# Kernel optimization log

Measured on AMD Instinct MI355X. Metric: run time of the kernel, lower is better.

## Reference

```python
import jax, jax.numpy as jnp
import numpy as np

IN_FEATURES = 256
OUT_FEATURES = 128
ALPHA = 0.2  # LeakyReLU negative slope
NEG_INF = -9e15
N_NODES = 8192


def _xavier_uniform(key, shape, gain):
    fan_in, fan_out = shape[0], shape[1]
    limit = gain * np.sqrt(6.0 / (fan_in + fan_out))
    return jax.random.uniform(key, shape, jnp.float32, -limit, limit)


def setup_inputs() -> dict:
    key = jax.random.key(0)
    k_h, k_adj, k_W, k_a = jax.random.split(key, 4)
    h = jax.random.normal(k_h, (N_NODES, IN_FEATURES), dtype=jnp.float32)
    adj = jax.random.randint(k_adj, (N_NODES, N_NODES), 0, 2, dtype=jnp.int32)
    W = _xavier_uniform(k_W, (IN_FEATURES, OUT_FEATURES), gain=1.414)
    a = _xavier_uniform(k_a, (2 * OUT_FEATURES, 1), gain=1.414)
    return {"h": h, "adj": adj, "W": W, "a": a}


def reference(h, adj, W, a):
    # Wh: (N, F_out)
    Wh = h @ W
    # Decompose a = [a1; a2]; e_ij = leakyrelu(Wh_i . a1 + Wh_j . a2)
    # == the original concat([Wh_i, Wh_j]) @ a, without the O(N^2*2F) tensor.
    a1 = a[:OUT_FEATURES, 0]  # (F_out,)
    a2 = a[OUT_FEATURES:, 0]  # (F_out,)
    src = Wh @ a1  # (N,)
    dst = Wh @ a2  # (N,)
    e = jax.nn.leaky_relu(src[:, None] + dst[None, :], negative_slope=ALPHA)  # (N, N)
    attention = jnp.where(adj > 0, e, NEG_INF)
    attention = jax.nn.softmax(attention, axis=1)
    # dropout p=0.0 (eval) -> identity
    h_prime = attention @ Wh  # (N, F_out)
    return jax.nn.elu(h_prime)  # concat=True
```

## Files before the change

kernel.cpp:

```cpp
#include <hip/hip_runtime.h>

#define N_NODES 8192
#define IN_F    256
#define OUT_F   128
#define ALPHA_S 0.2f

typedef __attribute__((ext_vector_type(8))) short  short8;
typedef __attribute__((ext_vector_type(4))) short  short4v;
typedef __attribute__((ext_vector_type(4))) float  floatx4;
typedef __attribute__((ext_vector_type(4))) int    intx4;
typedef __attribute__((ext_vector_type(4))) float  fx4;

static __device__ __forceinline__ float bf2f(short s) {
    union { unsigned int i; float f; } u;
    u.i = ((unsigned int)(unsigned short)s) << 16;
    return u.f;
}
static __device__ __forceinline__ short f2bf(float f) {
    union { float f; unsigned int i; } u; u.f = f;
    unsigned int r = u.i + 0x7FFFu + ((u.i >> 16) & 1u);
    return (short)(r >> 16);
}

__global__ __launch_bounds__(512) void k_wh(
    const float* __restrict__ h, const float* __restrict__ W,
    const float* __restrict__ a,
    short* __restrict__ WhB, float* __restrict__ src, float* __restrict__ dst)
{
    __shared__ short Wt[OUT_F][IN_F + 8];
    __shared__ short htile[32][IN_F + 8];
    __shared__ float q1s[IN_F], q2s[IN_F];
    __shared__ short wh_t[OUT_F][40];

    const int t      = threadIdx.x;
    const int lane   = t & 63;
    const int wave   = t >> 6;
    const int r_base = blockIdx.x * 32;

#pragma unroll
    for (int rep = 0; rep < 4; ++rep) {
        const int idx = rep * 8192 + t * 16;
        const int k   = idx >> 7;
        const int f   = idx & 127;
        fx4 w0 = *(const fx4*)(W + idx);
        fx4 w1 = *(const fx4*)(W + idx + 4);
        fx4 w2 = *(const fx4*)(W + idx + 8);
        fx4 w3 = *(const fx4*)(W + idx + 12);
        fx4 a10 = *(const fx4*)(a + f);
        fx4 a11 = *(const fx4*)(a + f + 4);
        fx4 a12 = *(const fx4*)(a + f + 8);
        fx4 a13 = *(const fx4*)(a + f + 12);
        fx4 a20 = *(const fx4*)(a + OUT_F + f);
        fx4 a21 = *(const fx4*)(a + OUT_F + f + 4);
        fx4 a22 = *(const fx4*)(a + OUT_F + f + 8);
        fx4 a23 = *(const fx4*)(a + OUT_F + f + 12);
        float p1 = 0.f, p2 = 0.f;
#pragma unroll
        for (int e = 0; e < 4; ++e) {
            p1 = fmaf(w0[e], a10[e], p1); p2 = fmaf(w0[e], a20[e], p2);
            p1 = fmaf(w1[e], a11[e], p1); p2 = fmaf(w1[e], a21[e], p2);
            p1 = fmaf(w2[e], a12[e], p1); p2 = fmaf(w2[e], a22[e], p2);
            p1 = fmaf(w3[e], a13[e], p1); p2 = fmaf(w3[e], a23[e], p2);
        }
#pragma unroll
        for (int e = 0; e < 4; ++e) {
            Wt[f + e][k]      = f2bf(w0[e]);
            Wt[f + 4 + e][k]  = f2bf(w1[e]);
            Wt[f + 8 + e][k]  = f2bf(w2[e]);
            Wt[f + 12 + e][k] = f2bf(w3[e]);
        }
#pragma unroll
        for (int m = 1; m < 8; m <<= 1) {
            p1 += __shfl_xor(p1, m, 64);
            p2 += __shfl_xor(p2, m, 64);
        }
        if ((t & 7) == 0) { q1s[k] = p1; q2s[k] = p2; }
    }

    const int r0   = t >> 4;
    const int fgrp = t & 15;
    const int k0   = fgrp * 16;
    fx4 h0, h1, h2, h3;
    {
        const float* hp = h + (size_t)(r_base + r0) * IN_F + k0;
        h0 = *(const fx4*)hp; h1 = *(const fx4*)(hp + 4);
        h2 = *(const fx4*)(hp + 8); h3 = *(const fx4*)(hp + 12);
        short8 b0, b1;
#pragma unroll
        for (int e = 0; e < 4; ++e) {
            b0[e]     = f2bf(h0[e]); b0[4 + e] = f2bf(h1[e]);
            b1[e]     = f2bf(h2[e]); b1[4 + e] = f2bf(h3[e]);
        }
        *(short8*)&htile[r0][k0]     = b0;
        *(short8*)&htile[r0][k0 + 8] = b1;
    }
    __syncthreads();

    {
        float sp = 0.f, dp = 0.f;
#pragma unroll
        for (int e = 0; e < 4; ++e) {
            sp = fmaf(h0[e], q1s[k0 + e], sp);      dp = fmaf(h0[e], q2s[k0 + e], dp);
            sp = fmaf(h1[e], q1s[k0 + 4 + e], sp);  dp = fmaf(h1[e], q2s[k0 + 4 + e], dp);
            sp = fmaf(h2[e], q1s[k0 + 8 + e], sp);  dp = fmaf(h2[e], q2s[k0 + 8 + e], dp);
            sp = fmaf(h3[e], q1s[k0 + 12 + e], sp); dp = fmaf(h3[e], q2s[k0 + 12 + e], dp);
        }
#pragma unroll
        for (int m = 1; m < 16; m <<= 1) {
            sp += __shfl_xor(sp, m, 64);
            dp += __shfl_xor(dp, m, 64);
        }
        if (fgrp == 0) { src[r_base + r0] = sp; dst[r_base + r0] = dp; }
    }

    const int ln15 = lane & 15;
    const int q    = lane >> 4;
    const int f0   = wave * 16;
    floatx4 c0 = {0.f, 0.f, 0.f, 0.f};
    floatx4 c1 = {0.f, 0.f, 0.f, 0.f};
#pragma unroll
    for (int s = 0; s < 8; ++s) {
        short8 bf  = *(const short8*)&Wt[f0 + ln15][s * 32 + q * 8];
        short8 a0f = *(const short8*)&htile[ln15][s * 32 + q * 8];
        short8 a1f = *(const short8*)&htile[16 + ln15][s * 32 + q * 8];
        c0 = __builtin_amdgcn_mfma_f32_16x16x32_bf16(a0f, bf, c0, 0, 0, 0);
        c1 = __builtin_amdgcn_mfma_f32_16x16x32_bf16(a1f, bf, c1, 0, 0, 0);
    }
    {
        short4v p0, p1;
#pragma unroll
        for (int r = 0; r < 4; ++r) { p0[r] = f2bf(c0[r]); p1[r] = f2bf(c1[r]); }
        *(short4v*)&wh_t[f0 + ln15][q * 4]      = p0;
        *(short4v*)&wh_t[f0 + ln15][16 + q * 4] = p1;
    }
    __syncthreads();
    {
        const int ft2 = t >> 6;
        const int l2  = t & 63;
        const int n2  = l2 & 15;
        const int q2  = l2 >> 4;
        short8 v = *(const short8*)&wh_t[ft2 * 16 + n2][q2 * 8];
        *(short8*)(WhB + (((size_t)blockIdx.x * 8 + ft2) * 64 + l2) * 8) = v;
    }
}

__global__ __launch_bounds__(256) void k_weights(
    const int*   __restrict__ adj,
    const float* __restrict__ src,
    const float* __restrict__ dstv,
    short* __restrict__ P,
    float* __restrict__ denom_part)
{
    __shared__ float wsum[4];
    const int bi  = blockIdx.x;
    const int row = bi >> 1;
    const int c0  = (bi & 1) * 4096;
    const int t   = threadIdx.x;
    const int col = c0 + t * 16;

    const float srow = src[row];
    const int*   ap = adj + (size_t)row * N_NODES + col;
    const float* dp = dstv + col;

    intx4 m[4]; fx4 d[4];
#pragma unroll
    for (int v = 0; v < 4; ++v) {
        m[v] = *(const intx4*)(ap + v * 4);
        d[v] = *(const fx4*)(dp + v * 4);
    }

    short8 w0, w1;
    float lsum = 0.f;
#pragma unroll
    for (int v = 0; v < 4; ++v) {
#pragma unroll
        for (int e = 0; e < 4; ++e) {
            float x = srow + d[v][e];
            float l = fmaxf(x, ALPHA_S * x);
            short b = (m[v][e] > 0) ? f2bf(__expf(l)) : (short)0;
            lsum += bf2f(b);
            if (v < 2) w0[v * 4 + e] = b;
            else       w1[(v - 2) * 4 + e] = b;
        }
    }
    short* pp = P + (size_t)row * N_NODES + col;
    *(short8*)pp       = w0;
    *(short8*)(pp + 8) = w1;

#pragma unroll
    for (int s = 1; s < 64; s <<= 1) lsum += __shfl_xor(lsum, s, 64);
    if ((t & 63) == 0) wsum[t >> 6] = lsum;
    __syncthreads();
    if (t == 0)
        denom_part[(size_t)(bi & 1) * N_NODES + row] =
            wsum[0] + wsum[1] + wsum[2] + wsum[3];
}

#define KSPLIT 8
#define KCH  (N_NODES / KSPLIT)
#define PBK  128
#define PSTR (PBK + 8)
#define PNIT (KCH / PBK)

__global__ __launch_bounds__(512) void k_pv(
    const short* __restrict__ P,
    const short* __restrict__ WhB,
    float* __restrict__ numer_part)
{
    __shared__ short atile[128 * PSTR];

    const int t    = threadIdx.x;
    const int lane = t & 63;
    const int wave = t >> 6;
    const int rg   = blockIdx.x >> 3;
    const int kc   = blockIdx.x & 7;
    const int r0   = rg * 128;
    const int kb   = kc * KCH;
    const int jb0  = kb >> 5;

    const int ln15 = lane & 15;
    const int q    = lane >> 4;

    const int srow2 = t >> 2;
    const int sc    = (t & 3) * 32;
    const short* pgl = P + (size_t)(r0 + srow2) * N_NODES + kb + sc;
    short* lw = &atile[srow2 * PSTR + sc];

    floatx4 acc[8];
#pragma unroll
    for (int rt = 0; rt < 8; ++rt) acc[rt] = (floatx4){0.f, 0.f, 0.f, 0.f};

    for (int it = 0; it < PNIT; ++it) {
        __syncthreads();
        {
            const short* pg = pgl + it * PBK;
#pragma unroll
            for (int u = 0; u < 4; ++u)
                *(short8*)(lw + u * 8) = *(const short8*)(pg + u * 8);
        }
        __syncthreads();
        const short* bbase = WhB + (((size_t)(jb0 + it * 4) * 8 + wave) * 64 + lane) * 8;
#pragma unroll
        for (int kf = 0; kf < 4; ++kf) {
            short8 Bf = *(const short8*)(bbase + (size_t)kf * 8 * 64 * 8);
#pragma unroll
            for (int rt = 0; rt < 8; ++rt) {
                short8 Af = *(const short8*)&atile[(rt * 16 + ln15) * PSTR + kf * 32 + q * 8];
                acc[rt] = __builtin_amdgcn_mfma_f32_16x16x32_bf16(Af, Bf, acc[rt], 0, 0, 0);
            }
        }
    }

    float* np = numer_part + ((size_t)kc * N_NODES + r0) * OUT_F + wave * 16 + ln15;
#pragma unroll
    for (int rt = 0; rt < 8; ++rt)
#pragma unroll
        for (int r = 0; r < 4; ++r)
            np[(size_t)(rt * 16 + q * 4 + r) * OUT_F] = acc[rt][r];
}

__global__ void k_final(const float* __restrict__ numer_part,
                        const float* __restrict__ denom_part,
                        float* __restrict__ out) {
    const int idx = blockIdx.x * 256 + threadIdx.x;
    const int row = idx >> 7;
    float v = 0.f;
#pragma unroll
    for (int kc = 0; kc < KSPLIT; ++kc)
        v += numer_part[(size_t)kc * N_NODES * OUT_F + idx];
    float dn = denom_part[row] + denom_part[N_NODES + row];
    v = (dn != 0.f) ? (v / dn) : 0.f;
    v = v > 0.f ? v : (__expf(v) - 1.f);
    out[idx] = v;
}

extern "C" void kernel_launch(void* const* d_in, const int* in_sizes, int n_in,
                              void* d_out, int out_size, void* d_ws, size_t ws_size,
                              hipStream_t stream) {
    const float* h   = (const float*)d_in[0];
    const int*   adj = (const int*)d_in[1];
    const float* W   = (const float*)d_in[2];
    const float* a   = (const float*)d_in[3];
    float* out = (float*)d_out;

    char*  ws         = (char*)d_ws;
    float* denom_part = (float*)ws;
    short* WhB        = (short*)(ws + (256 << 10));
    float* src        = (float*)(ws + (256 << 10) + (2 << 20));
    float* dst        = src + N_NODES;
    float* numer_part = (float*)(ws + (4 << 20));
    short* P          = (short*)(ws + (64ull << 20));

    k_wh      <<<256, 512, 0, stream>>>(h, W, a, WhB, src, dst);
    k_weights <<<16384, 256, 0, stream>>>(adj, src, dst, P, denom_part);
    k_pv      <<<512, 512, 0, stream>>>(P, WhB, numer_part);
    k_final   <<<4096, 256, 0, stream>>>(numer_part, denom_part, out);
}
```

Baseline: 441.9 us.

## Emit P in MFMA fragment layout and register-pipeline the PV matmul

k_weights now processes 16-row by 256-column tiles, staging bf16 weights through LDS and writing P directly in MFMA A-fragment order, with 32 partial denominators per row. k_pv drops its LDS tile and barriers: each wave loads pre-swizzled A and B fragments straight from global memory with double-buffered registers and computes a 32x128 output over one K-chunk. The aim is to remove LDS staging and synchronisation from the matmul and get fully coalesced fragment loads. In exchange there are more denominator partials to sum in k_final, more B reloads per wave, and higher register pressure.

```diff
diff --git a/kernel.cpp b/kernel.cpp
--- a/kernel.cpp
+++ b/kernel.cpp
@@ -148,115 +148,114 @@
     const int*   __restrict__ adj,
     const float* __restrict__ src,
     const float* __restrict__ dstv,
-    short* __restrict__ P,
+    short* __restrict__ Pfrag,
     float* __restrict__ denom_part)
 {
-    __shared__ float wsum[4];
-    const int bi  = blockIdx.x;
-    const int row = bi >> 1;
-    const int c0  = (bi & 1) * 4096;
-    const int t   = threadIdx.x;
-    const int col = c0 + t * 16;
-
-    const float srow = src[row];
-    const int*   ap = adj + (size_t)row * N_NODES + col;
-    const float* dp = dstv + col;
-
-    intx4 m[4]; fx4 d[4];
-#pragma unroll
-    for (int v = 0; v < 4; ++v) {
-        m[v] = *(const intx4*)(ap + v * 4);
-        d[v] = *(const fx4*)(dp + v * 4);
-    }
-
-    short8 w0, w1;
-    float lsum = 0.f;
-#pragma unroll
-    for (int v = 0; v < 4; ++v) {
-#pragma unroll
-        for (int e = 0; e < 4; ++e) {
-            float x = srow + d[v][e];
+    __shared__ short wl[16][264];
+
+    const int t    = threadIdx.x;
+    const int lane = t & 63;
+    const int wv   = t >> 6;
+    const int rt   = blockIdx.x >> 5;
+    const int cc   = blockIdx.x & 31;
+    const int jb   = cc * 256;
+
+    const fx4 dv = *(const fx4*)(dstv + jb + lane * 4);
+
+#pragma unroll
+    for (int p = 0; p < 4; ++p) {
+        const int rloc = p * 4 + wv;
+        const int row  = rt * 16 + rloc;
+        const float srow = src[row];
+        intx4 m = *(const intx4*)(adj + (size_t)row * N_NODES + jb + lane * 4);
+        short4v w;
+        float ls = 0.f;
+#pragma unroll
+        for (int e = 0; e < 4; ++e) {
+            float x = srow + dv[e];
             float l = fmaxf(x, ALPHA_S * x);
-            short b = (m[v][e] > 0) ? f2bf(__expf(l)) : (short)0;
-            lsum += bf2f(b);
-            if (v < 2) w0[v * 4 + e] = b;
-            else       w1[(v - 2) * 4 + e] = b;
-        }
-    }
-    short* pp = P + (size_t)row * N_NODES + col;
-    *(short8*)pp       = w0;
-    *(short8*)(pp + 8) = w1;
-
-#pragma unroll
-    for (int s = 1; s < 64; s <<= 1) lsum += __shfl_xor(lsum, s, 64);
-    if ((t & 63) == 0) wsum[t >> 6] = lsum;
+            short b = (m[e] > 0) ? f2bf(__expf(l)) : (short)0;
+            w[e] = b;
+            ls += bf2f(b);
+        }
+        *(short4v*)&wl[rloc][lane * 4] = w;
+#pragma unroll
+        for (int s = 1; s < 64; s <<= 1) ls += __shfl_xor(ls, s, 64);
+        if (lane == 0) denom_part[(size_t)cc * N_NODES + row] = ls;
+    }
     __syncthreads();
-    if (t == 0)
-        denom_part[(size_t)(bi & 1) * N_NODES + row] =
-            wsum[0] + wsum[1] + wsum[2] + wsum[3];
-}
-
-#define KSPLIT 8
-#define KCH  (N_NODES / KSPLIT)
-#define PBK  128
-#define PSTR (PBK + 8)
-#define PNIT (KCH / PBK)
-
-__global__ __launch_bounds__(512) void k_pv(
-    const short* __restrict__ P,
+
+    const int ln15 = lane & 15;
+    const int q    = lane >> 4;
+#pragma unroll
+    for (int p = 0; p < 2; ++p) {
+        const int kb = p * 4 + wv;
+        short8 v = *(const short8*)&wl[ln15][kb * 32 + q * 8];
+        *(short8*)(Pfrag + (((size_t)rt * 256) + (size_t)cc * 8 + kb) * 512
+                   + lane * 8) = v;
+    }
+}
+
+#define PVSPLIT 8
+__global__ __launch_bounds__(256, 2) void k_pv(
+    const short* __restrict__ Pfrag,
     const short* __restrict__ WhB,
     float* __restrict__ numer_part)
 {
-    __shared__ short atile[128 * PSTR];
-
     const int t    = threadIdx.x;
     const int lane = t & 63;
-    const int wave = t >> 6;
-    const int rg   = blockIdx.x >> 3;
-    const int kc   = blockIdx.x & 7;
-    const int r0   = rg * 128;
-    const int kb   = kc * KCH;
-    const int jb0  = kb >> 5;
+    const int wv   = t >> 6;
+    const int gw   = blockIdx.x * 4 + wv;
+    const int rp   = gw >> 3;
+    const int kc   = gw & 7;
+
+    const short* A0b = Pfrag + ((size_t)(rp * 2)     * 256) * 512 + lane * 8;
+    const short* A1b = Pfrag + ((size_t)(rp * 2 + 1) * 256) * 512 + lane * 8;
+    const short* Bb  = WhB + (size_t)lane * 8;
+
+    floatx4 acc[2][8];
+#pragma unroll
+    for (int pr = 0; pr < 2; ++pr)
+#pragma unroll
+        for (int ft = 0; ft < 8; ++ft) acc[pr][ft] = (floatx4){0.f, 0.f, 0.f, 0.f};
+
+    short8 A0[2], A1[2], B[2][8];
+
+    auto load = [&](int i, int ph) {
+        const size_t kblk = kc * 32 + i;
+        A0[ph] = *(const short8*)(A0b + kblk * 512);
+        A1[ph] = *(const short8*)(A1b + kblk * 512);
+#pragma unroll
+        for (int ft = 0; ft < 8; ++ft)
+            B[ph][ft] = *(const short8*)(Bb + (kblk * 8 + ft) * 512);
+    };
+    auto comp = [&](int ph) {
+#pragma unroll
+        for (int ft = 0; ft < 8; ++ft) {
+            acc[0][ft] = __builtin_amdgcn_mfma_f32_16x16x32_bf16(A0[ph], B[ph][ft], acc[0][ft], 0, 0, 0);
+            acc[1][ft] = __builtin_amdgcn_mfma_f32_16x16x32_bf16(A1[ph], B[ph][ft], acc[1][ft], 0, 0, 0);
+        }
+    };
+
+    load(0, 0);
+    for (int i = 0; i < 32; i += 2) {
+        if (i + 1 < 32) load(i + 1, 1);
+        comp(0);
+        if (i + 2 < 32) load(i + 2, 0);
+        comp(1);
+    }
 
     const int ln15 = lane & 15;
     const int q    = lane >> 4;
-
-    const int srow2 = t >> 2;
-    const int sc    = (t & 3) * 32;
-    const short* pgl = P + (size_t)(r0 + srow2) * N_NODES + kb + sc;
-    short* lw = &atile[srow2 * PSTR + sc];
-
-    floatx4 acc[8];
-#pragma unroll
-    for (int rt = 0; rt < 8; ++rt) acc[rt] = (floatx4){0.f, 0.f, 0.f, 0.f};
-
-    for (int it = 0; it < PNIT; ++it) {
-        __syncthreads();
-        {
-            const short* pg = pgl + it * PBK;
-#pragma unroll
-            for (int u = 0; u < 4; ++u)
-                *(short8*)(lw + u * 8) = *(const short8*)(pg + u * 8);
-        }
-        __syncthreads();
-        const short* bbase = WhB + (((size_t)(jb0 + it * 4) * 8 + wave) * 64 + lane) * 8;
-#pragma unroll
-        for (int kf = 0; kf < 4; ++kf) {
-            short8 Bf = *(const short8*)(bbase + (size_t)kf * 8 * 64 * 8);
-#pragma unroll
-            for (int rt = 0; rt < 8; ++rt) {
-                short8 Af = *(const short8*)&atile[(rt * 16 + ln15) * PSTR + kf * 32 + q * 8];
-                acc[rt] = __builtin_amdgcn_mfma_f32_16x16x32_bf16(Af, Bf, acc[rt], 0, 0, 0);
-            }
-        }
-    }
-
-    float* np = numer_part + ((size_t)kc * N_NODES + r0) * OUT_F + wave * 16 + ln15;
-#pragma unroll
-    for (int rt = 0; rt < 8; ++rt)
-#pragma unroll
-        for (int r = 0; r < 4; ++r)
-            np[(size_t)(rt * 16 + q * 4 + r) * OUT_F] = acc[rt][r];
+    float* np = numer_part + (size_t)kc * N_NODES * OUT_F;
+#pragma unroll
+    for (int pr = 0; pr < 2; ++pr)
+#pragma unroll
+        for (int ft = 0; ft < 8; ++ft)
+#pragma unroll
+            for (int r = 0; r < 4; ++r)
+                np[(size_t)(rp * 32 + pr * 16 + q * 4 + r) * OUT_F + ft * 16 + ln15]
+                    = acc[pr][ft][r];
 }
 
 __global__ void k_final(const float* __restrict__ numer_part,
@@ -266,9 +265,12 @@
     const int row = idx >> 7;
     float v = 0.f;
 #pragma unroll
-    for (int kc = 0; kc < KSPLIT; ++kc)
+    for (int kc = 0; kc < PVSPLIT; ++kc)
         v += numer_part[(size_t)kc * N_NODES * OUT_F + idx];
-    float dn = denom_part[row] + denom_part[N_NODES + row];
+    float dn = 0.f;
+#pragma unroll
+    for (int cc = 0; cc < 32; ++cc)
+        dn += denom_part[(size_t)cc * N_NODES + row];
     v = (dn != 0.f) ? (v / dn) : 0.f;
     v = v > 0.f ? v : (__expf(v) - 1.f);
     out[idx] = v;
@@ -285,14 +287,14 @@
 
     char*  ws         = (char*)d_ws;
     float* denom_part = (float*)ws;
-    short* WhB        = (short*)(ws + (256 << 10));
-    float* src        = (float*)(ws + (256 << 10) + (2 << 20));
+    short* WhB        = (short*)(ws + (1 << 20));
+    float* src        = (float*)(ws + (3 << 20));
     float* dst        = src + N_NODES;
     float* numer_part = (float*)(ws + (4 << 20));
-    short* P          = (short*)(ws + (64ull << 20));
+    short* Pfrag      = (short*)(ws + (64ull << 20));
 
     k_wh      <<<256, 512, 0, stream>>>(h, W, a, WhB, src, dst);
-    k_weights <<<16384, 256, 0, stream>>>(adj, src, dst, P, denom_part);
-    k_pv      <<<512, 512, 0, stream>>>(P, WhB, numer_part);
+    k_weights <<<16384, 256, 0, stream>>>(adj, src, dst, Pfrag, denom_part);
+    k_pv      <<<512, 256, 0, stream>>>(Pfrag, WhB, numer_part);
     k_final   <<<4096, 256, 0, stream>>>(numer_part, denom_part, out);
 }
```

Result: no change. 448.9 us (+1.6%).
